# Optimization experiments

Hardware: AMD Instinct MI355X
Metric: run time of the kernel (lower is better)

## Reference

```python
import jax, jax.numpy as jnp
import numpy as np

N_NODES = 8192
N_EDGES = 49152
IN_F, HID, H1, H2, OUT_F = 128, 64, 64, 5, 32
N_BONDS = 64


def setup_inputs() -> dict:
    key = jax.random.key(0)
    ks = jax.random.split(key, 12)
    s = 0.05
    return {
        "x": jax.random.normal(ks[0], (N_NODES, IN_F), jnp.float32),
        "edge_index": jax.random.randint(ks[1], (2, N_EDGES), 0, N_NODES, jnp.int32),
        "lefts": jax.random.randint(ks[2], (N_BONDS,), 0, N_NODES, jnp.int32),
        "rights": jax.random.randint(ks[3], (N_BONDS,), 0, N_NODES, jnp.int32),
        "W1": jax.random.normal(ks[4], (H1 * HID, IN_F), jnp.float32) * s,
        "att_src1": jax.random.normal(ks[5], (H1, HID), jnp.float32) * s,
        "att_dst1": jax.random.normal(ks[6], (H1, HID), jnp.float32) * s,
        "b1": jnp.zeros((H1 * HID,), jnp.float32),
        "W2": jax.random.normal(ks[7], (H2 * OUT_F, H1 * HID), jnp.float32) * s,
        "att_src2": jax.random.normal(ks[8], (H2, OUT_F), jnp.float32) * s,
        "att_dst2": jax.random.normal(ks[9], (H2, OUT_F), jnp.float32) * s,
        "b2": jnp.zeros((OUT_F,), jnp.float32),
    }


def _gat_conv(x, src, dst, W, a_src, a_dst, b, concat):
    # x: [N, F_in]; W: [H*C, F_in]; a_src/a_dst: [H, C]
    N = x.shape[0]
    H, C = a_src.shape
    h = (x @ W.T).reshape(N, H, C)                    # [N, H, C]
    alpha_s = jnp.einsum("nhc,hc->nh", h, a_src)      # [N, H]
    alpha_d = jnp.einsum("nhc,hc->nh", h, a_dst)
    logits = jax.nn.leaky_relu(alpha_s[src] + alpha_d[dst], negative_slope=0.2)  # [E, H]
    # scatter-softmax over incoming edges of each destination node
    m = jax.ops.segment_max(logits, dst, num_segments=N)
    e = jnp.exp(logits - m[dst])
    denom = jax.ops.segment_sum(e, dst, num_segments=N)
    alpha = e / denom[dst]                            # [E, H]
    msg = h[src] * alpha[:, :, None]                  # [E, H, C]
    out = jax.ops.segment_sum(msg, dst, num_segments=N)  # [N, H, C]
    out = out.reshape(N, H * C) if concat else out.mean(axis=1)
    return out + b


def reference(x, edge_index, lefts, rights, W1, att_src1, att_dst1, b1,
              W2, att_src2, att_dst2, b2):
    N = x.shape[0]
    loops = jnp.arange(N, dtype=edge_index.dtype)
    src = jnp.concatenate([edge_index[0], loops])
    dst = jnp.concatenate([edge_index[1], loops])
    x1 = jax.nn.elu(_gat_conv(x, src, dst, W1, att_src1, att_dst1, b1, concat=True))
    x2 = _gat_conv(x1, src, dst, W2, att_src2, att_dst2, b2, concat=False)  # [N, OUT_F]
    score = (x2[lefts] + x2[rights]).sum(axis=-1)     # [N_BONDS]
    return jax.nn.softmax(score, axis=0)
```

## Files before the change

### kernel.cpp

```cpp
#include <hip/hip_runtime.h>
#include <hip/hip_bf16.h>
#include <math.h>

#define N_NODES  8192
#define N_EDGES  49152
#define E_TOT    57344
#define IN_F     128
#define HID      64
#define NH1      64
#define NH2      5
#define OUT_F    32
#define F1       4096
#define F2       160
#define N_BONDS  64
#define ET       16
#define NP       4
#define HG       16

typedef short bf16x8 __attribute__((ext_vector_type(8)));
typedef float f32x4  __attribute__((ext_vector_type(4)));

__device__ __forceinline__ float lrelu(float x){ return x > 0.f ? x : 0.2f*x; }

__device__ __forceinline__ unsigned short bf16_rne(float f){
    unsigned u = __float_as_uint(f);
    unsigned r = u + 0x7FFF + ((u >> 16) & 1);
    return (unsigned short)(r >> 16);
}
__device__ __forceinline__ float bf16f(unsigned short h){
    return __uint_as_float((unsigned)h << 16);
}

__device__ __forceinline__ void block_sync_lds(){
    asm volatile("s_waitcnt lgkmcnt(0)" ::: "memory");
    __builtin_amdgcn_s_barrier();
    asm volatile("" ::: "memory");
}

__device__ __forceinline__ void gload_lds16(const unsigned short* gp, unsigned short* lp_base){
    __builtin_amdgcn_global_load_lds(
        (const __attribute__((address_space(1))) unsigned int*)(const void*)gp,
        (__attribute__((address_space(3))) unsigned int*)(void*)lp_base,
        16, 0, 0);
}

__global__ void k_count(const int* __restrict__ ei, int* counts){
    int i = blockIdx.x*256 + threadIdx.x;
    if (i < N_EDGES) atomicAdd(&counts[ei[N_EDGES + i]], 1);
}
__global__ __launch_bounds__(1024) void k_scan(const int* __restrict__ counts,
                                               int* __restrict__ row_start,
                                               int* __restrict__ cursor){
    __shared__ int sd[1024];
    int t = threadIdx.x;
    int v[8]; int sum = 0;
    #pragma unroll
    for (int i=0;i<8;i++){ v[i] = counts[t*8+i] + 1; sum += v[i]; }
    sd[t] = sum; __syncthreads();
    for (int off=1; off<1024; off<<=1){
        int vv = (t >= off) ? sd[t-off] : 0;
        __syncthreads();
        sd[t] += vv;
        __syncthreads();
    }
    int run = sd[t] - sum;
    #pragma unroll
    for (int i=0;i<8;i++){ row_start[t*8+i] = run; cursor[t*8+i] = run; run += v[i]; }
    if (t == 1023) row_start[N_NODES] = run;
}
__global__ void k_fill(const int* __restrict__ ei, int* cursor, int* __restrict__ csr_src){
    int i = blockIdx.x*256 + threadIdx.x;
    if (i >= E_TOT) return;
    int s, d;
    if (i < N_EDGES){ s = ei[i]; d = ei[N_EDGES + i]; }
    else { s = i - N_EDGES; d = s; }
    int pos = atomicAdd(&cursor[d], 1);
    csr_src[pos] = s;
}

__global__ __launch_bounds__(256) void k_prep(const float* __restrict__ W1,
        const float* __restrict__ W2,
        const float* __restrict__ a_s, const float* __restrict__ a_d,
        unsigned short* __restrict__ w1fh, unsigned short* __restrict__ w1fl,
        unsigned short* __restrict__ w2fh, unsigned short* __restrict__ w2fl,
        float* __restrict__ vv){
    int b = blockIdx.x, t = threadIdx.x;
    if (b < 256){
        int g = b*256 + t;
        int lane = g & 63, ct = (g >> 6) & 3, ks = (g >> 8) & 3, hg = g >> 10;
        int col = hg*64 + ct*16 + (lane & 15);
        int k = ks*32 + (lane >> 4)*8;
        const float* src = W1 + (size_t)col*IN_F + k;
        bf16x8 hv, lv;
        #pragma unroll
        for (int j=0;j<8;j++){
            float f = src[j];
            unsigned short hb = bf16_rne(f);
            hv[j] = (short)hb;
            lv[j] = (short)bf16_rne(f - bf16f(hb));
        }
        *(bf16x8*)(w1fh + (size_t)g*8) = hv;
        *(bf16x8*)(w1fl + (size_t)g*8) = lv;
    } else if (b < 576){
        int g = (b-256)*256 + t;
        int lane = g & 63, ni = (g >> 6) % 10, kc = g / 640;
        int n = ni*16 + (lane & 15);
        int k = kc*32 + (lane >> 4)*8;
        const float* src = W2 + (size_t)n*F1 + k;
        bf16x8 hv, lv;
        #pragma unroll
        for (int j=0;j<8;j++){
            float f = src[j];
            unsigned short hb = bf16_rne(f);
            hv[j] = (short)hb;
            lv[j] = (short)bf16_rne(f - bf16f(hb));
        }
        *(bf16x8*)(w2fh + (size_t)g*8) = hv;
        *(bf16x8*)(w2fl + (size_t)g*8) = lv;
    } else {
        int idx = (b-576)*256 + t;
        int j = idx >> 7, k = idx & 127;
        int h = j & 63;
        const float* ap = (j < 64) ? a_s : a_d;
        float s = 0.f;
        for (int c = 0; c < HID; c++)
            s += ap[h*HID + c] * W1[(size_t)(h*HID + c)*IN_F + k];
        vv[k*128 + j] = s;
    }
}

__global__ __launch_bounds__(128) void k_alpha1x(const float* __restrict__ x,
        const float* __restrict__ vv,
        float* __restrict__ as1, float* __restrict__ ad1){
    int b = blockIdx.x, t = threadIdx.x;
    __shared__ float xs[4][IN_F];
    int n0 = b*4;
    {
        int r = t >> 5, c4 = t & 31;
        *(float4*)&xs[r][c4*4] = *(const float4*)(x + (size_t)(n0+r)*IN_F + c4*4);
    }
    __syncthreads();
    float a0=0.f, a1=0.f, a2=0.f, a3=0.f;
    #pragma unroll 4
    for (int k=0;k<IN_F;k++){
        float v = vv[k*128 + t];
        a0 += xs[0][k]*v; a1 += xs[1][k]*v; a2 += xs[2][k]*v; a3 += xs[3][k]*v;
    }
    int hd = t & 63;
    float* outp = (t < 64) ? as1 : ad1;
    outp[(n0+0)*NH1 + hd] = a0;
    outp[(n0+1)*NH1 + hd] = a1;
    outp[(n0+2)*NH1 + hd] = a2;
    outp[(n0+3)*NH1 + hd] = a3;
}

__global__ __launch_bounds__(256) void k_aggx64(const float* __restrict__ x,
        const float* __restrict__ as1, const float* __restrict__ ad1,
        const int* __restrict__ row_start, const int* __restrict__ csr_src,
        unsigned short* __restrict__ txhi){
    int n = blockIdx.x, t = threadIdx.x;
    __shared__ float ad_s[NH1];
    __shared__ float wt[ET][NH1];
    __shared__ int   st[ET];
    __shared__ float xs[ET][IN_F];
    int e0 = row_start[n], e1 = row_start[n+1];
    if (t < NH1) ad_s[t] = ad1[n*NH1 + t];
    int hq = t >> 4, f0 = (t & 15)*8;
    float acc[4][8] = {};
    float D[4] = {0.f, 0.f, 0.f, 0.f};
    for (int eb = e0; eb < e1; eb += ET){
        int ne = min(ET, e1 - eb);
        if (t < ne) st[t] = csr_src[eb + t];
        __syncthreads();
        for (int idx = t; idx < ne*32; idx += 256){
            int e = idx >> 5, f4 = idx & 31;
            *(float4*)&xs[e][f4*4] = *(const float4*)(x + (size_t)st[e]*IN_F + f4*4);
        }
        for (int idx = t; idx < ne*NH1; idx += 256){
            int e = idx >> 6, hh = idx & 63;
            wt[e][hh] = __expf(lrelu(as1[st[e]*NH1 + hh] + ad_s[hh]));
        }
        __syncthreads();
        for (int e = 0; e < ne; e++){
            float4 v0 = *(const float4*)&xs[e][f0];
            float4 v1 = *(const float4*)&xs[e][f0+4];
            float xv[8] = {v0.x,v0.y,v0.z,v0.w,v1.x,v1.y,v1.z,v1.w};
            #pragma unroll
            for (int c=0;c<4;c++){
                float w = wt[e][hq*4 + c];
                D[c] += w;
                #pragma unroll
                for (int j=0;j<8;j++) acc[c][j] += w*xv[j];
            }
        }
        __syncthreads();
    }
    #pragma unroll
    for (int c=0;c<4;c++){
        float dinv = 1.f / D[c];
        bf16x8 hv;
        #pragma unroll
        for (int j=0;j<8;j++) hv[j] = (short)bf16_rne(acc[c][j] * dinv);
        size_t o = ((size_t)(hq*4 + c)*N_NODES + n)*IN_F + f0;
        *(bf16x8*)(txhi + o) = hv;
    }
}

__global__ __launch_bounds__(512, 4) void k_gemm12(
        const unsigned short* __restrict__ txhi,
        const unsigned short* __restrict__ w1fh, const unsigned short* __restrict__ w1fl,
        const unsigned short* __restrict__ w2fh, const unsigned short* __restrict__ w2fl,
        const float* __restrict__ b1,
        float* __restrict__ P){
    __shared__ __attribute__((aligned(16))) unsigned short Als[8192];
    __shared__ __attribute__((aligned(16))) unsigned short W1sh[8192];
    __shared__ __attribute__((aligned(16))) unsigned short W2s[20480];
    __shared__ __attribute__((aligned(16))) unsigned short X1s[4096];

    const int tid  = threadIdx.x;
    const int wave = tid >> 6, lane = tid & 63;
    const int wr = wave & 1, wc = wave >> 1;
    const int q = lane >> 4, l16 = lane & 15;
    const int row0 = blockIdx.x * 64;
    const int g = blockIdx.y;
    const int h0 = g * HG;
    const int nbase = (wc < 2) ? wc*3 : 6 + (wc-2)*2;

    {
        const unsigned short* Ab = txhi + ((size_t)h0*N_NODES + row0)*IN_F;
        const unsigned short* W1b = w1fh + (size_t)h0*8192;
        #pragma unroll
        for (int j=0;j<2;j++){
            int idx = j*8 + wave;
            int eo = idx*512 + lane*8;
            int row = eo >> 7;
            int se = (eo & ~127) | ((eo & 127) ^ ((row & 7) << 3));
            gload_lds16(Ab + se, &Als[idx*512]);
        }
        #pragma unroll
        for (int j=0;j<2;j++){
            int idx = j*8 + wave;
            gload_lds16(W1b + idx*512 + lane*8, &W1sh[idx*512]);
        }
    }

    f32x4 acc2[2][3] = {};
    bf16x8 wlo[4];

    #pragma unroll 1
    for (int hh = 0; hh < HG; hh++){
        const int h = h0 + hh;
        block_sync_lds();
        {
            const unsigned short* W1lb = w1fl + (size_t)h*8192;
            #pragma unroll
            for (int ks=0;ks<4;ks++)
                wlo[ks] = *(const bf16x8*)(W1lb + (size_t)(ks*4 + wc)*512 + lane*8);
        }
        asm volatile("" ::: "memory");
        {
            const unsigned short* W2bh = w2fh + (size_t)h*10240;
            const unsigned short* W2bl = w2fl + (size_t)h*10240;
            #pragma unroll
            for (int j=0;j<5;j++){
                int idx = j*8 + wave;
                const unsigned short* src = (idx < 20) ? (W2bh + idx*512 + lane*8)
                                                       : (W2bl + (idx-20)*512 + lane*8);
                gload_lds16(src, &W2s[idx*512]);
            }
        }
        asm volatile("s_waitcnt vmcnt(9)" ::: "memory");
        __builtin_amdgcn_s_barrier();
        f32x4 c1[2] = {};
        __builtin_amdgcn_s_setprio(1);
        #pragma unroll
        for (int ks=0;ks<4;ks++){
            bf16x8 bh = *(const bf16x8*)&W1sh[(ks*4 + wc)*512 + lane*8];
            #pragma unroll
            for (int mi=0;mi<2;mi++){
                int arow = wr*32 + mi*16 + l16;
                int sidx = (arow*128 + ks*32 + q*8) ^ ((arow & 7) << 3);
                bf16x8 af = *(const bf16x8*)&Als[sidx];
                c1[mi] = __builtin_amdgcn_mfma_f32_16x16x32_bf16(af, bh, c1[mi], 0,0,0);
                c1[mi] = __builtin_amdgcn_mfma_f32_16x16x32_bf16(af, wlo[ks], c1[mi], 0,0,0);
            }
        }
        __builtin_amdgcn_s_setprio(0);
        {
            int col = wc*16 + l16;
            float b = b1[h*64 + col];
            #pragma unroll
            for (int mi=0;mi<2;mi++){
                #pragma unroll
                for (int i=0;i<4;i++){
                    float v = c1[mi][i] + b;
                    float o = v > 0.f ? v : (__expf(v) - 1.f);
                    int row = wr*32 + mi*16 + q*4 + i;
                    int sidx = (row*64 + col) ^ ((row & 7) << 3);
                    X1s[sidx] = bf16_rne(o);
                }
            }
        }
        asm volatile("s_waitcnt vmcnt(0) lgkmcnt(0)" ::: "memory");
        __builtin_amdgcn_s_barrier();
        if (hh + 1 < HG){
            const unsigned short* Ab = txhi + ((size_t)(h+1)*N_NODES + row0)*IN_F;
            const unsigned short* W1b = w1fh + (size_t)(h+1)*8192;
            #pragma unroll
            for (int j=0;j<2;j++){
                int idx = j*8 + wave;
                int eo = idx*512 + lane*8;
                int row = eo >> 7;
                int se = (eo & ~127) | ((eo & 127) ^ ((row & 7) << 3));
                gload_lds16(Ab + se, &Als[idx*512]);
            }
            #pragma unroll
            for (int j=0;j<2;j++){
                int idx = j*8 + wave;
                gload_lds16(W1b + idx*512 + lane*8, &W1sh[idx*512]);
            }
        }
        __builtin_amdgcn_s_setprio(1);
        #pragma unroll
        for (int ks=0;ks<2;ks++){
            bf16x8 a2[2];
            #pragma unroll
            for (int mi=0;mi<2;mi++){
                int row = wr*32 + mi*16 + l16;
                int sidx = (row*64 + ks*32 + q*8) ^ ((row & 7) << 3);
                a2[mi] = *(const bf16x8*)&X1s[sidx];
            }
            if (wc < 2){
                #pragma unroll
                for (int ni=0;ni<3;ni++){
                    int f = (ks*10 + nbase + ni)*512 + lane*8;
                    bf16x8 bh = *(const bf16x8*)&W2s[f];
                    bf16x8 bl = *(const bf16x8*)&W2s[10240 + f];
                    #pragma unroll
                    for (int mi=0;mi<2;mi++){
                        acc2[mi][ni] = __builtin_amdgcn_mfma_f32_16x16x32_bf16(a2[mi], bh, acc2[mi][ni], 0,0,0);
                        acc2[mi][ni] = __builtin_amdgcn_mfma_f32_16x16x32_bf16(a2[mi], bl, acc2[mi][ni], 0,0,0);
                    }
                }
            } else {
                #pragma unroll
                for (int ni=0;ni<2;ni++){
                    int f = (ks*10 + nbase + ni)*512 + lane*8;
                    bf16x8 bh = *(const bf16x8*)&W2s[f];
                    bf16x8 bl = *(const bf16x8*)&W2s[10240 + f];
                    #pragma unroll
                    for (int mi=0;mi<2;mi++){
                        acc2[mi][ni] = __builtin_amdgcn_mfma_f32_16x16x32_bf16(a2[mi], bh, acc2[mi][ni], 0,0,0);
                        acc2[mi][ni] = __builtin_amdgcn_mfma_f32_16x16x32_bf16(a2[mi], bl, acc2[mi][ni], 0,0,0);
                    }
                }
            }
        }
        __builtin_amdgcn_s_setprio(0);
    }

    float* outp = P + ((size_t)g*N_NODES + row0)*F2;
    #pragma unroll
    for (int mi=0;mi<2;mi++)
        #pragma unroll
        for (int ni=0;ni<3;ni++){
            if (wc >= 2 && ni >= 2) continue;
            #pragma unroll
            for (int i=0;i<4;i++){
                int rr = wr*32 + mi*16 + q*4 + i;
                int cc = (nbase + ni)*16 + l16;
                outp[(size_t)rr*F2 + cc] = acc2[mi][ni][i];
            }
        }
}

__global__ __launch_bounds__(256) void k_redalpha(const float* __restrict__ P,
        const float* __restrict__ att_s, const float* __restrict__ att_d,
        float* __restrict__ h2, float* __restrict__ as2, float* __restrict__ ad2){
    __shared__ float hs[32][164];
    __shared__ float avs[160], avd[160];
    int b = blockIdx.x, t = threadIdx.x;
    int n0 = b*32;
    if (t < 160){ avs[t] = att_s[t]; avd[t] = att_d[t]; }
    const int NV = N_NODES*F2/4;
    int base = b * (32*F2/4);
    #pragma unroll
    for (int v=0; v<5; v++){
        int i = base + v*256 + t;
        float4 a = ((const float4*)P)[i];
        #pragma unroll
        for (int kb=1; kb<NP; kb++){
            float4 bb = ((const float4*)P)[(size_t)kb*NV + i];
            a.x+=bb.x; a.y+=bb.y; a.z+=bb.z; a.w+=bb.w;
        }
        ((float4*)h2)[i] = a;
        int flat = (v*256 + t)*4;
        int n = flat / F2, c = flat % F2;
        *(float4*)&hs[n][c] = a;
    }
    __syncthreads();
    if (t < 160){
        int n = t/5, hh = t%5;
        const float* hp = &hs[n][hh*32];
        const float* ap = &avs[hh*32];
        const float* dp = &avd[hh*32];
        float s=0.f, d=0.f;
        #pragma unroll
        for (int c=0;c<32;c++){ float hv=hp[c]; s += hv*ap[c]; d += hv*dp[c]; }
        as2[(n0+n)*NH2 + hh] = s;
        ad2[(n0+n)*NH2 + hh] = d;
    }
}

__global__ __launch_bounds__(192) void k_agg2(const float* __restrict__ h2,
        const float* __restrict__ as2, const float* __restrict__ ad2,
        const int* __restrict__ row_start, const int* __restrict__ csr_src,
        const float* __restrict__ b2, float* __restrict__ x2){
    int n = blockIdx.x, t = threadIdx.x;
    __shared__ float ad_s[NH2], sacc[F2];
    int e0 = row_start[n], e1 = row_start[n+1];
    if (t < NH2) ad_s[t] = ad2[n*NH2 + t];
    __syncthreads();
    if (t < F2){
        int h = t >> 5;
        float adh = ad_s[h];
        float acc = 0.f, D = 0.f;
        for (int e=e0;e<e1;e++){
            int s = csr_src[e];
            float w = __expf(lrelu(as2[s*NH2 + h] + adh));
            acc += w * h2[(size_t)s*F2 + t];
            D += w;
        }
        sacc[t] = acc / D;
    }
    __syncthreads();
    if (t < OUT_F){
        float v = (sacc[t] + sacc[t+32] + sacc[t+64] + sacc[t+96] + sacc[t+128]) * 0.2f + b2[t];
        x2[n*OUT_F + t] = v;
    }
}

__global__ __launch_bounds__(64) void k_bond(const float* __restrict__ x2,
        const int* __restrict__ lefts, const int* __restrict__ rights,
        float* __restrict__ out){
    int b = threadIdx.x;
    int L = lefts[b], R = rights[b];
    float s = 0.f;
    #pragma unroll
    for (int c=0;c<OUT_F;c+=4){
        float4 l4 = *(const float4*)(x2 + (size_t)L*OUT_F + c);
        float4 r4 = *(const float4*)(x2 + (size_t)R*OUT_F + c);
        s += l4.x+l4.y+l4.z+l4.w + r4.x+r4.y+r4.z+r4.w;
    }
    float m = s;
    #pragma unroll
    for (int off=1; off<64; off<<=1) m = fmaxf(m, __shfl_xor(m, off));
    float e = expf(s - m);
    float sum = e;
    #pragma unroll
    for (int off=1; off<64; off<<=1) sum += __shfl_xor(sum, off);
    out[b] = e / sum;
}

extern "C" void kernel_launch(void* const* d_in, const int* in_sizes, int n_in,
                              void* d_out, int out_size, void* d_ws, size_t ws_size,
                              hipStream_t stream){
    const float* x      = (const float*)d_in[0];
    const int*   ei     = (const int*)  d_in[1];
    const int*   lefts  = (const int*)  d_in[2];
    const int*   rights = (const int*)  d_in[3];
    const float* W1     = (const float*)d_in[4];
    const float* att_s1 = (const float*)d_in[5];
    const float* att_d1 = (const float*)d_in[6];
    const float* b1     = (const float*)d_in[7];
    const float* W2     = (const float*)d_in[8];
    const float* att_s2 = (const float*)d_in[9];
    const float* att_d2 = (const float*)d_in[10];
    const float* b2     = (const float*)d_in[11];
    float* out = (float*)d_out;

    char* ws = (char*)d_ws;
    size_t off = 0;
    auto alloc = [&](size_t bytes) -> void* {
        void* p = ws + off;
        off += (bytes + 255) & ~(size_t)255;
        return p;
    };
    unsigned short* txhi = (unsigned short*)alloc((size_t)NH1*N_NODES*IN_F*2);
    float* part   = (float*)alloc((size_t)NP*N_NODES*F2*4);
    float* h2     = (float*)alloc((size_t)N_NODES*F2*4);
    float* as1    = (float*)alloc((size_t)N_NODES*NH1*4);
    float* ad1    = (float*)alloc((size_t)N_NODES*NH1*4);
    float* as2    = (float*)alloc((size_t)N_NODES*NH2*4);
    float* ad2    = (float*)alloc((size_t)N_NODES*NH2*4);
    float* x2     = (float*)alloc((size_t)N_NODES*OUT_F*4);
    float* vv     = (float*)alloc((size_t)IN_F*128*4);
    unsigned short* w1fh = (unsigned short*)alloc((size_t)F1*IN_F*2);
    unsigned short* w1fl = (unsigned short*)alloc((size_t)F1*IN_F*2);
    unsigned short* w2fh = (unsigned short*)alloc((size_t)128*10*512*2);
    unsigned short* w2fl = (unsigned short*)alloc((size_t)128*10*512*2);
    int* counts    = (int*)alloc((size_t)N_NODES*4);
    int* row_start = (int*)alloc((size_t)(N_NODES+1)*4);
    int* cursor    = (int*)alloc((size_t)N_NODES*4);
    int* csr_src   = (int*)alloc((size_t)E_TOT*4);

    hipMemsetAsync(counts, 0, (size_t)N_NODES*4, stream);
    k_count<<<192, 256, 0, stream>>>(ei, counts);
    k_scan<<<1, 1024, 0, stream>>>(counts, row_start, cursor);
    k_fill<<<224, 256, 0, stream>>>(ei, cursor, csr_src);

    k_prep<<<640, 256, 0, stream>>>(W1, W2, att_s1, att_d1,
                                    w1fh, w1fl, w2fh, w2fl, vv);

    k_alpha1x<<<N_NODES/4, 128, 0, stream>>>(x, vv, as1, ad1);

    k_aggx64<<<N_NODES, 256, 0, stream>>>(x, as1, ad1, row_start, csr_src, txhi);

    k_gemm12<<<dim3(128, NP), 512, 0, stream>>>(txhi, w1fh, w1fl, w2fh, w2fl, b1, part);
    k_redalpha<<<256, 256, 0, stream>>>(part, att_s2, att_d2, h2, as2, ad2);

    k_agg2<<<N_NODES, 192, 0, stream>>>(h2, as2, ad2, row_start, csr_src, b2, x2);

    k_bond<<<1, 64, 0, stream>>>(x2, lefts, rights, out);
}
```

Measured before the change: 210.7 us.

## Load W2 fragments into registers and double-buffer X1 to drop a barrier

The fused GEMM kernel no longer stages W2 through shared memory. Each wave loads its own W2 hi/lo fragments straight from global memory into registers. X1 is double-buffered in LDS, which removes one of the two per-iteration block barriers and lets the next head's A/W1 prefetch start earlier, with vmcnt waits retuned to match. The aim is less LDS traffic and fewer syncs per head, at the cost of more VGPRs and redundant global loads of W2 across blocks. The hand-counted waitcnt values risk being wrong.

New measurement: 337.1 us. 60.0% more time.

```diff
diff --git a/kernel.cpp b/kernel.cpp
--- a/kernel.cpp
+++ b/kernel.cpp
@@ -214,8 +214,7 @@
         float* __restrict__ P){
     __shared__ __attribute__((aligned(16))) unsigned short Als[8192];
     __shared__ __attribute__((aligned(16))) unsigned short W1sh[8192];
-    __shared__ __attribute__((aligned(16))) unsigned short W2s[20480];
-    __shared__ __attribute__((aligned(16))) unsigned short X1s[4096];
+    __shared__ __attribute__((aligned(16))) unsigned short X1s[8192];
 
     const int tid  = threadIdx.x;
     const int wave = tid >> 6, lane = tid & 63;
@@ -245,31 +244,43 @@
     }
 
     f32x4 acc2[2][3] = {};
-    bf16x8 wlo[4];
+    bf16x8 wlo[4], w2h[3][2], w2l[3][2];
 
     #pragma unroll 1
     for (int hh = 0; hh < HG; hh++){
         const int h = h0 + hh;
-        block_sync_lds();
+        const int xb = (hh & 1) ? 4096 : 0;
+        const int col = wc*16 + l16;
+        float bb = b1[h*64 + col];
         {
             const unsigned short* W1lb = w1fl + (size_t)h*8192;
             #pragma unroll
             for (int ks=0;ks<4;ks++)
                 wlo[ks] = *(const bf16x8*)(W1lb + (size_t)(ks*4 + wc)*512 + lane*8);
         }
-        asm volatile("" ::: "memory");
         {
-            const unsigned short* W2bh = w2fh + (size_t)h*10240;
-            const unsigned short* W2bl = w2fl + (size_t)h*10240;
-            #pragma unroll
-            for (int j=0;j<5;j++){
-                int idx = j*8 + wave;
-                const unsigned short* src = (idx < 20) ? (W2bh + idx*512 + lane*8)
-                                                       : (W2bl + (idx-20)*512 + lane*8);
-                gload_lds16(src, &W2s[idx*512]);
-            }
-        }
-        asm volatile("s_waitcnt vmcnt(9)" ::: "memory");
+            const unsigned short* W2bh = w2fh + (size_t)h*10240 + lane*8;
+            const unsigned short* W2bl = w2fl + (size_t)h*10240 + lane*8;
+            if (wc < 2){
+                #pragma unroll
+                for (int ni=0;ni<3;ni++)
+                    #pragma unroll
+                    for (int ks=0;ks<2;ks++){
+                        w2h[ni][ks] = *(const bf16x8*)(W2bh + (size_t)(ks*10 + nbase + ni)*512);
+                        w2l[ni][ks] = *(const bf16x8*)(W2bl + (size_t)(ks*10 + nbase + ni)*512);
+                    }
+            } else {
+                #pragma unroll
+                for (int ni=0;ni<2;ni++)
+                    #pragma unroll
+                    for (int ks=0;ks<2;ks++){
+                        w2h[ni][ks] = *(const bf16x8*)(W2bh + (size_t)(ks*10 + nbase + ni)*512);
+                        w2l[ni][ks] = *(const bf16x8*)(W2bl + (size_t)(ks*10 + nbase + ni)*512);
+                    }
+            }
+        }
+        if (wc < 2) asm volatile("s_waitcnt vmcnt(17)" ::: "memory");
+        else        asm volatile("s_waitcnt vmcnt(13)" ::: "memory");
         __builtin_amdgcn_s_barrier();
         f32x4 c1[2] = {};
         __builtin_amdgcn_s_setprio(1);
@@ -286,26 +297,22 @@
             }
         }
         __builtin_amdgcn_s_setprio(0);
+        #pragma unroll
+        for (int mi=0;mi<2;mi++){
+            #pragma unroll
+            for (int i=0;i<4;i++){
+                float v = c1[mi][i] + bb;
+                float o = v > 0.f ? v : (__expf(v) - 1.f);
+                int row = wr*32 + mi*16 + q*4 + i;
+                int sidx = xb + ((row*64 + col) ^ ((row & 7) << 3));
+                X1s[sidx] = bf16_rne(o);
+            }
+        }
+        block_sync_lds();
         {
-            int col = wc*16 + l16;
-            float b = b1[h*64 + col];
-            #pragma unroll
-            for (int mi=0;mi<2;mi++){
-                #pragma unroll
-                for (int i=0;i<4;i++){
-                    float v = c1[mi][i] + b;
-                    float o = v > 0.f ? v : (__expf(v) - 1.f);
-                    int row = wr*32 + mi*16 + q*4 + i;
-                    int sidx = (row*64 + col) ^ ((row & 7) << 3);
-                    X1s[sidx] = bf16_rne(o);
-                }
-            }
-        }
-        asm volatile("s_waitcnt vmcnt(0) lgkmcnt(0)" ::: "memory");
-        __builtin_amdgcn_s_barrier();
-        if (hh + 1 < HG){
-            const unsigned short* Ab = txhi + ((size_t)(h+1)*N_NODES + row0)*IN_F;
-            const unsigned short* W1b = w1fh + (size_t)(h+1)*8192;
+            const int hn = (hh + 1 < HG) ? (h + 1) : h;
+            const unsigned short* Ab = txhi + ((size_t)hn*N_NODES + row0)*IN_F;
+            const unsigned short* W1b = w1fh + (size_t)hn*8192;
             #pragma unroll
             for (int j=0;j<2;j++){
                 int idx = j*8 + wave;
@@ -320,6 +327,7 @@
                 gload_lds16(W1b + idx*512 + lane*8, &W1sh[idx*512]);
             }
         }
+        asm volatile("s_waitcnt vmcnt(4)" ::: "memory");
         __builtin_amdgcn_s_setprio(1);
         #pragma unroll
         for (int ks=0;ks<2;ks++){
@@ -327,33 +335,25 @@
             #pragma unroll
             for (int mi=0;mi<2;mi++){
                 int row = wr*32 + mi*16 + l16;
-                int sidx = (row*64 + ks*32 + q*8) ^ ((row & 7) << 3);
+                int sidx = xb + ((row*64 + ks*32 + q*8) ^ ((row & 7) << 3));
                 a2[mi] = *(const bf16x8*)&X1s[sidx];
             }
             if (wc < 2){
                 #pragma unroll
-                for (int ni=0;ni<3;ni++){
-                    int f = (ks*10 + nbase + ni)*512 + lane*8;
-                    bf16x8 bh = *(const bf16x8*)&W2s[f];
-                    bf16x8 bl = *(const bf16x8*)&W2s[10240 + f];
+                for (int ni=0;ni<3;ni++)
                     #pragma unroll
                     for (int mi=0;mi<2;mi++){
-                        acc2[mi][ni] = __builtin_amdgcn_mfma_f32_16x16x32_bf16(a2[mi], bh, acc2[mi][ni], 0,0,0);
-                        acc2[mi][ni] = __builtin_amdgcn_mfma_f32_16x16x32_bf16(a2[mi], bl, acc2[mi][ni], 0,0,0);
+                        acc2[mi][ni] = __builtin_amdgcn_mfma_f32_16x16x32_bf16(a2[mi], w2h[ni][ks], acc2[mi][ni], 0,0,0);
+                        acc2[mi][ni] = __builtin_amdgcn_mfma_f32_16x16x32_bf16(a2[mi], w2l[ni][ks], acc2[mi][ni], 0,0,0);
                     }
-                }
             } else {
                 #pragma unroll
-                for (int ni=0;ni<2;ni++){
-                    int f = (ks*10 + nbase + ni)*512 + lane*8;
-                    bf16x8 bh = *(const bf16x8*)&W2s[f];
-                    bf16x8 bl = *(const bf16x8*)&W2s[10240 + f];
+                for (int ni=0;ni<2;ni++)
                     #pragma unroll
                     for (int mi=0;mi<2;mi++){
-                        acc2[mi][ni] = __builtin_amdgcn_mfma_f32_16x16x32_bf16(a2[mi], bh, acc2[mi][ni], 0,0,0);
-                        acc2[mi][ni] = __builtin_amdgcn_mfma_f32_16x16x32_bf16(a2[mi], bl, acc2[mi][ni], 0,0,0);
+                        acc2[mi][ni] = __builtin_amdgcn_mfma_f32_16x16x32_bf16(a2[mi], w2h[ni][ks], acc2[mi][ni], 0,0,0);
+                        acc2[mi][ni] = __builtin_amdgcn_mfma_f32_16x16x32_bf16(a2[mi], w2l[ni][ks], acc2[mi][ni], 0,0,0);
                     }
-                }
             }
         }
         __builtin_amdgcn_s_setprio(0);
```
